# Kernel optimization log

Measured on AMD Instinct MI355X. Metric: run time of the kernel, lower is better.

The kernel has to match this reference:

```python
import jax, jax.numpy as jnp
import numpy as np

D = 256          # in_dim == hidden_dim (input_proj is Identity)
N_NODES = 17     # 1 center + 16 neighbors, full (all-to-all) graph
BATCH = 16384
NUM_LAYERS = 2
LN_EPS = 1e-5
LEAKY_SLOPE = 0.01  # nn.LeakyReLU default


def _sage_layer(h, W_l, b_l, W_r, ln_g, ln_b):
    """One _SAGELayer: SAGEConv(normalize=False) -> LayerNorm -> LeakyReLU.

    h: [b, n, d]. Full all-to-all topology (no self loops), so
    mean over neighbors = (sum over all nodes - self) / (n - 1),
    which is exactly what PyG's scatter-mean computes on this edge_index.
    SAGEConv: out = lin_l(mean_neigh) + lin_r(h)  (lin_l has bias, lin_r none).
    Dropout is inference-mode (identity).
    """
    n = h.shape[1]
    mean_neigh = (jnp.sum(h, axis=1, keepdims=True) - h) / (n - 1)  # [b,n,d]
    c = (jnp.einsum('bnd,od->bno', mean_neigh, W_l) + b_l
         + jnp.einsum('bnd,od->bno', h, W_r))                        # [b,n,d]
    mu = jnp.mean(c, axis=-1, keepdims=True)
    var = jnp.mean(jnp.square(c - mu), axis=-1, keepdims=True)
    y = (c - mu) * jax.lax.rsqrt(var + LN_EPS) * ln_g + ln_b
    a = jnp.where(y > 0, y, LEAKY_SLOPE * y)
    return a + h  # residual


def setup_inputs() -> dict:
    key = jax.random.key(0)
    ks = jax.random.split(key, 1 + 5 * NUM_LAYERS)
    inp = {"x": jax.random.normal(ks[0], (BATCH, N_NODES, D), dtype=jnp.float32)}
    scale = 1.0 / np.sqrt(D)
    for i in range(NUM_LAYERS):
        k0, k1, k2, k3, k4 = ks[1 + 5 * i: 6 + 5 * i]
        inp[f"W_l_{i}"] = jax.random.uniform(k0, (D, D), jnp.float32, -scale, scale)
        inp[f"b_l_{i}"] = jnp.zeros((D,), jnp.float32)
        inp[f"W_r_{i}"] = jax.random.uniform(k1, (D, D), jnp.float32, -scale, scale)
        inp[f"ln_g_{i}"] = jnp.ones((D,), jnp.float32)
        inp[f"ln_b_{i}"] = jnp.zeros((D,), jnp.float32)
    return inp


def reference(x, W_l_0, b_l_0, W_r_0, ln_g_0, ln_b_0,
              W_l_1, b_l_1, W_r_1, ln_g_1, ln_b_1):
    h = x  # input_proj is Identity (in_dim == hidden_dim)
    h = _sage_layer(h, W_l_0, b_l_0, W_r_0, ln_g_0, ln_b_0)
    h = _sage_layer(h, W_l_1, b_l_1, W_r_1, ln_g_1, ln_b_1)
    return h  # [b, n_nodes, hidden_dim]
```

## Files before the change

kernel.cpp:

```cpp
#include <hip/hip_runtime.h>

typedef unsigned short u16;
typedef unsigned int u32;
typedef __attribute__((ext_vector_type(8))) short bf16x8;
typedef __attribute__((ext_vector_type(4))) float f32x4;

#define D 256
#define NODES 17
#define NBATCH 16384
#define G 6
#define THREADS 512
#define WELEMS 65536

#define LDS_AH   0
#define LDS_AL   65536
#define LDS_T    131072
#define LDS_PART 138240
#define LDS_MURS 145408
#define LDS_TOTAL 146304

__device__ __forceinline__ float bf2f(u16 u) {
  union { float f; u32 i; } v; v.i = ((u32)u) << 16; return v.f;
}
__device__ __forceinline__ u16 f2bf(float f) {
  union { float f; u32 i; } v; v.f = f;
  u32 r = v.i + 0x7fffu + ((v.i >> 16) & 1u);
  return (u16)(r >> 16);
}
__device__ __forceinline__ u32 swz(int row, int byteInRow) {
  return (u32)(row * 512 + (byteInRow ^ ((row & 7) << 4)));
}

__global__ void prep_weights(const float* __restrict__ wl0, const float* __restrict__ wr0,
                             const float* __restrict__ wl1, const float* __restrict__ wr1,
                             u16* __restrict__ wc_hi, u16* __restrict__ wc_lo,
                             u16* __restrict__ wl_hi, u16* __restrict__ wl_lo) {
  int idx = blockIdx.x * 256 + threadIdx.x;
  int layer = idx >> 16;
  int e = idx & 65535;
  const float* wl = layer ? wl1 : wl0;
  const float* wr = layer ? wr1 : wr0;
  float l16 = wl[e] * 0.0625f;
  float wc = wr[e] - l16;
  u16 ch = f2bf(wc);
  wc_hi[idx] = ch;
  wc_lo[idx] = f2bf(wc - bf2f(ch));
  u16 lh = f2bf(l16);
  wl_hi[idx] = lh;
  wl_lo[idx] = f2bf(l16 - bf2f(lh));
}

__global__ __launch_bounds__(THREADS, 2) void sage_fused(
    const float* __restrict__ x,
    const float* __restrict__ bl0, const float* __restrict__ g0, const float* __restrict__ bt0,
    const float* __restrict__ bl1, const float* __restrict__ g1, const float* __restrict__ bt1,
    const u16* __restrict__ wc_hi, const u16* __restrict__ wc_lo,
    const u16* __restrict__ wl_hi, const u16* __restrict__ wl_lo,
    float* __restrict__ out) {
  extern __shared__ __align__(16) char smem[];
  float* T = (float*)(smem + LDS_T);
  float* PART = (float*)(smem + LDS_PART);
  float* MURS = (float*)(smem + LDS_MURS);

  const int tid = threadIdx.x;
  const int wave = tid >> 6;
  const int lane = tid & 63;
  const int l15 = lane & 15;
  const int hk = lane >> 4;
  const int b0 = blockIdx.x * G;
  const int geff = min(G, NBATCH - b0);
  const int vrows = geff * NODES;
  const size_t gbase = (size_t)b0 * NODES * D;
  const int colA = wave * 32 + l15;
  const int colB = colA + 16;

  for (int i = tid; i < vrows * 64; i += THREADS) {
    int r = i >> 6;
    int c4 = (i & 63) << 2;
    float4 v = *(const float4*)(x + gbase + (size_t)r * D + c4);
    u16 h0 = f2bf(v.x), h1 = f2bf(v.y), h2 = f2bf(v.z), h3 = f2bf(v.w);
    u16 q0 = f2bf(v.x - bf2f(h0)), q1 = f2bf(v.y - bf2f(h1));
    u16 q2 = f2bf(v.z - bf2f(h2)), q3 = f2bf(v.w - bf2f(h3));
    u32 off = swz(r, c4 * 2);
    *(uint2*)(smem + LDS_AH + off) =
        make_uint2((u32)h0 | ((u32)h1 << 16), (u32)h2 | ((u32)h3 << 16));
    *(uint2*)(smem + LDS_AL + off) =
        make_uint2((u32)q0 | ((u32)q1 << 16), (u32)q2 | ((u32)q3 << 16));
  }
  for (int i = vrows * 64 + tid; i < 128 * 64; i += THREADS) {
    int r = i >> 6;
    int c4 = (i & 63) << 2;
    u32 off = swz(r, c4 * 2);
    *(uint2*)(smem + LDS_AH + off) = make_uint2(0u, 0u);
    *(uint2*)(smem + LDS_AL + off) = make_uint2(0u, 0u);
  }
  __syncthreads();

#pragma unroll 1
  for (int layer = 0; layer < 2; ++layer) {
    const float* bl = layer ? bl1 : bl0;
    const float* lg = layer ? g1 : g0;
    const float* lb = layer ? bt1 : bt0;
    const u16* WCH = wc_hi + layer * WELEMS;
    const u16* WCL = wc_lo + layer * WELEMS;
    const u16* WLH = wl_hi + layer * WELEMS;
    const u16* WLL = wl_lo + layer * WELEMS;
    const float blA = bl[colA], blB = bl[colB];
    const float gA = lg[colA], gB = lg[colB];
    const float lbA = lb[colA], lbB = lb[colB];

    for (int p = tid; p < geff * 128; p += THREADS) {
      int d2 = (p & 127) << 1;
      int b = p >> 7;
      int rb = b * NODES;
      float s0 = 0.f, s1 = 0.f;
#pragma unroll
      for (int n = 0; n < NODES; ++n) {
        u32 off = swz(rb + n, d2 * 2);
        u32 vh = *(const u32*)(smem + LDS_AH + off);
        u32 vl = *(const u32*)(smem + LDS_AL + off);
        s0 += bf2f((u16)vh) + bf2f((u16)vl);
        s1 += bf2f((u16)(vh >> 16)) + bf2f((u16)(vl >> 16));
      }
      u16 h0 = f2bf(s0), h1 = f2bf(s1);
      u16 q0 = f2bf(s0 - bf2f(h0)), q1 = f2bf(s1 - bf2f(h1));
      u32 off = swz(112 + b, d2 * 2);
      *(u32*)(smem + LDS_AH + off) = (u32)h0 | ((u32)h1 << 16);
      *(u32*)(smem + LDS_AL + off) = (u32)q0 | ((u32)q1 << 16);
    }
    __syncthreads();

    f32x4 acc[7][2];
    f32x4 accS[2];
#pragma unroll
    for (int m = 0; m < 7; ++m)
#pragma unroll
      for (int nt = 0; nt < 2; ++nt) acc[m][nt] = (f32x4){0.f, 0.f, 0.f, 0.f};
    accS[0] = (f32x4){0.f, 0.f, 0.f, 0.f};
    accS[1] = (f32x4){0.f, 0.f, 0.f, 0.f};

#pragma unroll 2
    for (int k = 0; k < 8; ++k) {
      int kb = k * 32;
      bf16x8 bch[2], bcl[2];
#pragma unroll
      for (int nt = 0; nt < 2; ++nt) {
        size_t widx = (size_t)(colA + nt * 16) * 256 + kb + hk * 8;
        bch[nt] = *(const bf16x8*)(WCH + widx);
        bcl[nt] = *(const bf16x8*)(WCL + widx);
      }
#pragma unroll
      for (int m = 0; m < 7; ++m) {
        u32 off = swz(m * 16 + l15, kb * 2 + hk * 16);
        bf16x8 a_hi = *(const bf16x8*)(smem + LDS_AH + off);
        bf16x8 a_lo = *(const bf16x8*)(smem + LDS_AL + off);
#pragma unroll
        for (int nt = 0; nt < 2; ++nt) {
          acc[m][nt] = __builtin_amdgcn_mfma_f32_16x16x32_bf16(a_hi, bch[nt], acc[m][nt], 0, 0, 0);
          acc[m][nt] = __builtin_amdgcn_mfma_f32_16x16x32_bf16(a_hi, bcl[nt], acc[m][nt], 0, 0, 0);
          acc[m][nt] = __builtin_amdgcn_mfma_f32_16x16x32_bf16(a_lo, bch[nt], acc[m][nt], 0, 0, 0);
        }
      }
      {
        u32 off = swz(112 + l15, kb * 2 + hk * 16);
        bf16x8 a_hi = *(const bf16x8*)(smem + LDS_AH + off);
        bf16x8 a_lo = *(const bf16x8*)(smem + LDS_AL + off);
#pragma unroll
        for (int nt = 0; nt < 2; ++nt) {
          size_t widx = (size_t)(colA + nt * 16) * 256 + kb + hk * 8;
          bf16x8 bh = *(const bf16x8*)(WLH + widx);
          bf16x8 bq = *(const bf16x8*)(WLL + widx);
          accS[nt] = __builtin_amdgcn_mfma_f32_16x16x32_bf16(a_hi, bh, accS[nt], 0, 0, 0);
          accS[nt] = __builtin_amdgcn_mfma_f32_16x16x32_bf16(a_hi, bq, accS[nt], 0, 0, 0);
          accS[nt] = __builtin_amdgcn_mfma_f32_16x16x32_bf16(a_lo, bh, accS[nt], 0, 0, 0);
        }
      }
    }

#pragma unroll
    for (int nt = 0; nt < 2; ++nt)
#pragma unroll
      for (int j = 0; j < 4; ++j) {
        int b = hk * 4 + j;
        if (b < 7) T[b * 256 + colA + nt * 16] = accS[nt][j];
      }
    __syncthreads();

#pragma unroll
    for (int m = 0; m < 7; ++m) {
#pragma unroll
      for (int j = 0; j < 4; ++j) {
        int r = m * 16 + hk * 4 + j;
        int b = (r * 241) >> 12;
        b = b > 6 ? 6 : b;
        float c0 = acc[m][0][j] + T[b * 256 + colA] + blA;
        float c1 = acc[m][1][j] + T[b * 256 + colB] + blB;
        acc[m][0][j] = c0;
        acc[m][1][j] = c1;
        float ss = c0 + c1;
        float qq = c0 * c0 + c1 * c1;
#pragma unroll
        for (int msk = 1; msk < 16; msk <<= 1) {
          ss += __shfl_xor(ss, msk);
          qq += __shfl_xor(qq, msk);
        }
        if (l15 == 0) {
          PART[(r * 8 + wave) * 2] = ss;
          PART[(r * 8 + wave) * 2 + 1] = qq;
        }
      }
    }
    __syncthreads();

    if (tid < 112) {
      float ss = 0.f, qq = 0.f;
#pragma unroll
      for (int w = 0; w < 8; ++w) {
        ss += PART[(tid * 8 + w) * 2];
        qq += PART[(tid * 8 + w) * 2 + 1];
      }
      float mu = ss * 0.00390625f;
      float var = qq * 0.00390625f - mu * mu;
      MURS[tid * 2] = mu;
      MURS[tid * 2 + 1] = rsqrtf(var + 1e-5f);
    }
    __syncthreads();

#pragma unroll
    for (int m = 0; m < 7; ++m) {
#pragma unroll
      for (int j = 0; j < 4; ++j) {
        int r = m * 16 + hk * 4 + j;
        if (r < vrows) {
          float mu = MURS[r * 2];
          float rs = MURS[r * 2 + 1];
#pragma unroll
          for (int nt = 0; nt < 2; ++nt) {
            int col = colA + nt * 16;
            float y = (acc[m][nt][j] - mu) * rs * (nt ? gB : gA) + (nt ? lbB : lbA);
            float av = y > 0.f ? y : 0.01f * y;
            u32 off = swz(r, col * 2);
            float hold = bf2f(*(const u16*)(smem + LDS_AH + off)) +
                         bf2f(*(const u16*)(smem + LDS_AL + off));
            float o = av + hold;
            if (layer == 0) {
              u16 oh = f2bf(o);
              *(u16*)(smem + LDS_AH + off) = oh;
              *(u16*)(smem + LDS_AL + off) = f2bf(o - bf2f(oh));
            } else {
              out[gbase + (size_t)r * D + col] = o;
            }
          }
        }
      }
    }
    __syncthreads();
  }
}

extern "C" void kernel_launch(void* const* d_in, const int* in_sizes, int n_in,
                              void* d_out, int out_size, void* d_ws, size_t ws_size,
                              hipStream_t stream) {
  const float* x   = (const float*)d_in[0];
  const float* wl0 = (const float*)d_in[1];
  const float* bl0 = (const float*)d_in[2];
  const float* wr0 = (const float*)d_in[3];
  const float* g0  = (const float*)d_in[4];
  const float* bt0 = (const float*)d_in[5];
  const float* wl1 = (const float*)d_in[6];
  const float* bl1 = (const float*)d_in[7];
  const float* wr1 = (const float*)d_in[8];
  const float* g1  = (const float*)d_in[9];
  const float* bt1 = (const float*)d_in[10];

  u16* ws = (u16*)d_ws;
  u16* wch = ws;
  u16* wcl = ws + 2 * WELEMS;
  u16* wlh = ws + 4 * WELEMS;
  u16* wll = ws + 6 * WELEMS;

  prep_weights<<<512, 256, 0, stream>>>(wl0, wr0, wl1, wr1, wch, wcl, wlh, wll);

  hipFuncSetAttribute((const void*)sage_fused,
                      hipFuncAttributeMaxDynamicSharedMemorySize, LDS_TOTAL);
  int grid = (NBATCH + G - 1) / G;
  sage_fused<<<grid, THREADS, LDS_TOTAL, stream>>>(
      x, bl0, g0, bt0, bl1, g1, bt1, wch, wcl, wlh, wll, (float*)d_out);
}
```

Measured before the change: 1.678 ms.

## Split GEMM row tiles across 16 waves with 1024-thread blocks

Doubles the block to 1024 threads and splits the eight 16-row M tiles between two wave groups, so each wave holds 4 accumulator tiles instead of 7 plus the sum tile. The second group computes the batch-sum tile with the W_l weights in place of its fourth tile. This cuts per-wave register pressure and serial MFMA chains and adds more waves for latency hiding. In exchange, weight fragments are loaded by twice as many waves, the k-loop is no longer unrolled, and occupancy remains limited by LDS use of about 143 KB per block.

After: 1.788 ms. +6.5%, slower.

```diff
diff --git a/kernel.cpp b/kernel.cpp
--- a/kernel.cpp
+++ b/kernel.cpp
@@ -9,7 +9,7 @@
 #define NODES 17
 #define NBATCH 16384
 #define G 6
-#define THREADS 512
+#define THREADS 1024
 #define WELEMS 65536
 
 #define LDS_AH   0
@@ -50,7 +50,7 @@
   wl_lo[idx] = f2bf(l16 - bf2f(lh));
 }
 
-__global__ __launch_bounds__(THREADS, 2) void sage_fused(
+__global__ __launch_bounds__(THREADS, 4) void sage_fused(
     const float* __restrict__ x,
     const float* __restrict__ bl0, const float* __restrict__ g0, const float* __restrict__ bt0,
     const float* __restrict__ bl1, const float* __restrict__ g1, const float* __restrict__ bt1,
@@ -64,6 +64,8 @@
 
   const int tid = threadIdx.x;
   const int wave = tid >> 6;
+  const int wn = wave & 7;
+  const int wm = wave >> 3;
   const int lane = tid & 63;
   const int l15 = lane & 15;
   const int hk = lane >> 4;
@@ -71,7 +73,7 @@
   const int geff = min(G, NBATCH - b0);
   const int vrows = geff * NODES;
   const size_t gbase = (size_t)b0 * NODES * D;
-  const int colA = wave * 32 + l15;
+  const int colA = wn * 32 + l15;
   const int colB = colA + 16;
 
   for (int i = tid; i < vrows * 64; i += THREADS) {
@@ -130,73 +132,73 @@
     }
     __syncthreads();
 
-    f32x4 acc[7][2];
-    f32x4 accS[2];
-#pragma unroll
-    for (int m = 0; m < 7; ++m)
-#pragma unroll
-      for (int nt = 0; nt < 2; ++nt) acc[m][nt] = (f32x4){0.f, 0.f, 0.f, 0.f};
-    accS[0] = (f32x4){0.f, 0.f, 0.f, 0.f};
-    accS[1] = (f32x4){0.f, 0.f, 0.f, 0.f};
-
-#pragma unroll 2
+    f32x4 acc[4][2];
+#pragma unroll
+    for (int mt = 0; mt < 4; ++mt)
+#pragma unroll
+      for (int nt = 0; nt < 2; ++nt) acc[mt][nt] = (f32x4){0.f, 0.f, 0.f, 0.f};
+
+#pragma unroll 1
     for (int k = 0; k < 8; ++k) {
       int kb = k * 32;
-      bf16x8 bch[2], bcl[2];
+      bf16x8 bch[2], bcl[2], b3h[2], b3l[2];
 #pragma unroll
       for (int nt = 0; nt < 2; ++nt) {
         size_t widx = (size_t)(colA + nt * 16) * 256 + kb + hk * 8;
         bch[nt] = *(const bf16x8*)(WCH + widx);
         bcl[nt] = *(const bf16x8*)(WCL + widx);
       }
-#pragma unroll
-      for (int m = 0; m < 7; ++m) {
-        u32 off = swz(m * 16 + l15, kb * 2 + hk * 16);
+      if (wm) {
+#pragma unroll
+        for (int nt = 0; nt < 2; ++nt) {
+          size_t widx = (size_t)(colA + nt * 16) * 256 + kb + hk * 8;
+          b3h[nt] = *(const bf16x8*)(WLH + widx);
+          b3l[nt] = *(const bf16x8*)(WLL + widx);
+        }
+      } else {
+#pragma unroll
+        for (int nt = 0; nt < 2; ++nt) { b3h[nt] = bch[nt]; b3l[nt] = bcl[nt]; }
+      }
+#pragma unroll
+      for (int mt = 0; mt < 4; ++mt) {
+        u32 off = swz(wm * 64 + mt * 16 + l15, kb * 2 + hk * 16);
         bf16x8 a_hi = *(const bf16x8*)(smem + LDS_AH + off);
         bf16x8 a_lo = *(const bf16x8*)(smem + LDS_AL + off);
 #pragma unroll
         for (int nt = 0; nt < 2; ++nt) {
-          acc[m][nt] = __builtin_amdgcn_mfma_f32_16x16x32_bf16(a_hi, bch[nt], acc[m][nt], 0, 0, 0);
-          acc[m][nt] = __builtin_amdgcn_mfma_f32_16x16x32_bf16(a_hi, bcl[nt], acc[m][nt], 0, 0, 0);
-          acc[m][nt] = __builtin_amdgcn_mfma_f32_16x16x32_bf16(a_lo, bch[nt], acc[m][nt], 0, 0, 0);
-        }
-      }
-      {
-        u32 off = swz(112 + l15, kb * 2 + hk * 16);
-        bf16x8 a_hi = *(const bf16x8*)(smem + LDS_AH + off);
-        bf16x8 a_lo = *(const bf16x8*)(smem + LDS_AL + off);
-#pragma unroll
-        for (int nt = 0; nt < 2; ++nt) {
-          size_t widx = (size_t)(colA + nt * 16) * 256 + kb + hk * 8;
-          bf16x8 bh = *(const bf16x8*)(WLH + widx);
-          bf16x8 bq = *(const bf16x8*)(WLL + widx);
-          accS[nt] = __builtin_amdgcn_mfma_f32_16x16x32_bf16(a_hi, bh, accS[nt], 0, 0, 0);
-          accS[nt] = __builtin_amdgcn_mfma_f32_16x16x32_bf16(a_hi, bq, accS[nt], 0, 0, 0);
-          accS[nt] = __builtin_amdgcn_mfma_f32_16x16x32_bf16(a_lo, bh, accS[nt], 0, 0, 0);
-        }
-      }
-    }
-
-#pragma unroll
-    for (int nt = 0; nt < 2; ++nt)
+          bf16x8 bh = (mt == 3) ? b3h[nt] : bch[nt];
+          bf16x8 bq = (mt == 3) ? b3l[nt] : bcl[nt];
+          acc[mt][nt] = __builtin_amdgcn_mfma_f32_16x16x32_bf16(a_hi, bh, acc[mt][nt], 0, 0, 0);
+          acc[mt][nt] = __builtin_amdgcn_mfma_f32_16x16x32_bf16(a_hi, bq, acc[mt][nt], 0, 0, 0);
+          acc[mt][nt] = __builtin_amdgcn_mfma_f32_16x16x32_bf16(a_lo, bh, acc[mt][nt], 0, 0, 0);
+        }
+      }
+    }
+
+    if (wm == 1) {
+#pragma unroll
+      for (int nt = 0; nt < 2; ++nt)
+#pragma unroll
+        for (int j = 0; j < 4; ++j) {
+          int b = hk * 4 + j;
+          if (b < 7) T[b * 256 + colA + nt * 16] = acc[3][nt][j];
+        }
+    }
+    __syncthreads();
+
+#pragma unroll
+    for (int mt = 0; mt < 4; ++mt) {
+      int tile = wm * 4 + mt;
+      if (tile == 7) continue;
 #pragma unroll
       for (int j = 0; j < 4; ++j) {
-        int b = hk * 4 + j;
-        if (b < 7) T[b * 256 + colA + nt * 16] = accS[nt][j];
-      }
-    __syncthreads();
-
-#pragma unroll
-    for (int m = 0; m < 7; ++m) {
-#pragma unroll
-      for (int j = 0; j < 4; ++j) {
-        int r = m * 16 + hk * 4 + j;
+        int r = tile * 16 + hk * 4 + j;
         int b = (r * 241) >> 12;
         b = b > 6 ? 6 : b;
-        float c0 = acc[m][0][j] + T[b * 256 + colA] + blA;
-        float c1 = acc[m][1][j] + T[b * 256 + colB] + blB;
-        acc[m][0][j] = c0;
-        acc[m][1][j] = c1;
+        float c0 = acc[mt][0][j] + T[b * 256 + colA] + blA;
+        float c1 = acc[mt][1][j] + T[b * 256 + colB] + blB;
+        acc[mt][0][j] = c0;
+        acc[mt][1][j] = c1;
         float ss = c0 + c1;
         float qq = c0 * c0 + c1 * c1;
 #pragma unroll
@@ -205,8 +207,8 @@
           qq += __shfl_xor(qq, msk);
         }
         if (l15 == 0) {
-          PART[(r * 8 + wave) * 2] = ss;
-          PART[(r * 8 + wave) * 2 + 1] = qq;
+          PART[(r * 8 + wn) * 2] = ss;
+          PART[(r * 8 + wn) * 2 + 1] = qq;
         }
       }
     }
@@ -227,17 +229,19 @@
     __syncthreads();
 
 #pragma unroll
-    for (int m = 0; m < 7; ++m) {
+    for (int mt = 0; mt < 4; ++mt) {
+      int tile = wm * 4 + mt;
+      if (tile == 7) continue;
 #pragma unroll
       for (int j = 0; j < 4; ++j) {
-        int r = m * 16 + hk * 4 + j;
+        int r = tile * 16 + hk * 4 + j;
         if (r < vrows) {
           float mu = MURS[r * 2];
           float rs = MURS[r * 2 + 1];
 #pragma unroll
           for (int nt = 0; nt < 2; ++nt) {
             int col = colA + nt * 16;
-            float y = (acc[m][nt][j] - mu) * rs * (nt ? gB : gA) + (nt ? lbB : lbA);
+            float y = (acc[mt][nt][j] - mu) * rs * (nt ? gB : gA) + (nt ? lbB : lbA);
             float av = y > 0.f ? y : 0.01f * y;
             u32 off = swz(r, col * 2);
             float hold = bf2f(*(const u16*)(smem + LDS_AH + off)) +
```
